# Kernel tuning notes

Hardware: AMD Instinct MI355X
Metric: run time of the kernel (lower is better)

Reference implementation:

```python
import jax, jax.numpy as jnp
import numpy as np

BN_EPS = 1e-5


def setup_inputs() -> dict:
    key = jax.random.key(0)
    ks = jax.random.split(key, 12)
    N, F, H, E, ED, G, EMB = 59392, 116, 256, 950272, 5, 8, 16
    return {
        "x": jax.random.normal(ks[0], (N, F), dtype=jnp.float32),
        "edge_index": jax.random.randint(ks[1], (2, E), 0, N, dtype=jnp.int64),
        "edge_attr": jax.random.normal(ks[2], (E, ED), dtype=jnp.float32),
        "group_ids": jax.random.randint(ks[3], (N,), 0, G, dtype=jnp.int64),
        "group_emb": jax.random.normal(ks[4], (G, EMB), dtype=jnp.float32),
        "W_in": jax.random.normal(ks[5], (F + EMB, H), dtype=jnp.float32) * 0.05,
        "b_in": jnp.zeros((H,), dtype=jnp.float32),
        "gamma": jnp.ones((H,), dtype=jnp.float32),
        "beta": jnp.zeros((H,), dtype=jnp.float32),
        "We": jax.random.normal(ks[6], (ED, H), dtype=jnp.float32) * 0.05,
        "be": jnp.zeros((H,), dtype=jnp.float32),
        "W1": jax.random.normal(ks[7], (H, H), dtype=jnp.float32) * 0.05,
        "b1": jnp.zeros((H,), dtype=jnp.float32),
        "W2": jax.random.normal(ks[8], (H, H), dtype=jnp.float32) * 0.05,
        "b2": jnp.zeros((H,), dtype=jnp.float32),
    }


def reference(x, edge_index, edge_attr, group_ids, group_emb, W_in, b_in,
              gamma, beta, We, be, W1, b1, W2, b2):
    N = x.shape[0]
    # group-embedding concat (dropout is identity in eval mode)
    h = jnp.concatenate([x, group_emb[group_ids]], axis=-1)      # [N, F+EMB]
    # dynamically-created Linear + ReLU
    h = jax.nn.relu(h @ W_in + b_in)                              # [N, H]
    # BatchNorm over nodes (training stats, biased var)
    mu = jnp.mean(h, axis=0)
    var = jnp.mean(jnp.square(h - mu), axis=0)
    h = (h - mu) * jax.lax.rsqrt(var + BN_EPS) * gamma + beta
    # GINEConv: msg = ReLU(x_j + lin(edge_attr)); sum-aggregate at target
    src, dst = edge_index[0], edge_index[1]
    msg = jax.nn.relu(h[src] + edge_attr @ We + be)               # [E, H]
    agg = jax.ops.segment_sum(msg, dst, num_segments=N)          # [N, H]
    z = h + agg                                                   # (1+eps)*h, eps=0
    out = jax.nn.relu(z @ W1 + b1) @ W2 + b2                      # 2-layer MLP
    out = jax.nn.relu(out)
    return (out, edge_attr)
```

## Files before the change

kernel.cpp:

```cpp
#include <hip/hip_runtime.h>
#include <hip/hip_bf16.h>
#include <cstdint>
#include <cstddef>

#define H 256
#define EMB 16
#define ED 5
#define BN_EPS 1e-5f
#define CAP 48

typedef __attribute__((ext_vector_type(8))) short short8;
typedef __attribute__((ext_vector_type(4))) float f32x4;
typedef _Float16 h2 __attribute__((ext_vector_type(2)));

__device__ __forceinline__ unsigned short f2bf(float f) {
  unsigned int u = __float_as_uint(f);
  unsigned int r = (u + 0x7fffu + ((u >> 16) & 1u)) >> 16;
  return (unsigned short)r;
}
__device__ __forceinline__ unsigned int pk2bf(float a, float b) {
  return (unsigned int)f2bf(a) | ((unsigned int)f2bf(b) << 16);
}
__device__ __forceinline__ unsigned short f2h(float f) {
  union { _Float16 h; unsigned short u; } c;
  c.h = (_Float16)f;
  return c.u;
}
__device__ __forceinline__ h2 u2h2(unsigned int u) {
  union { unsigned int u; h2 h; } c;
  c.u = u;
  return c.h;
}
__device__ __forceinline__ unsigned int h22u(h2 h) {
  union { h2 h; unsigned int u; } c;
  c.h = h;
  return c.u;
}
__device__ __forceinline__ h2 mkh2(float a, float b) {
  h2 r;
  r.x = (_Float16)a;
  r.y = (_Float16)b;
  return r;
}

__global__ __launch_bounds__(256) void prep_kernel(
    const float* __restrict__ Win, const float* __restrict__ W1,
    const float* __restrict__ W2, const float* __restrict__ gemb,
    const float* __restrict__ b_in, unsigned short* __restrict__ Wtx,
    unsigned short* __restrict__ Wt1, unsigned short* __restrict__ Wt2,
    float* __restrict__ T, float* __restrict__ stats, int* __restrict__ cnt,
    int N, int F, int G) {
  int idx = blockIdx.x * 256 + threadIdx.x;
  if (idx < 1024) stats[idx] = 0.f;
  if (idx < N) cnt[idx] = 0;
  if (idx < 256 * 128) {
    int n = idx >> 7, k = idx & 127;
    Wtx[idx] = f2bf((k < F) ? Win[(size_t)k * H + n] : 0.f);
  } else if (idx < 256 * 128 + 65536) {
    int i2 = idx - 256 * 128;
    int n = i2 >> 8, k = i2 & 255;
    Wt1[i2] = f2bf(W1[(size_t)k * H + n]);
  } else if (idx < 256 * 128 + 131072) {
    int i2 = idx - 256 * 128 - 65536;
    int n = i2 >> 8, k = i2 & 255;
    Wt2[i2] = f2bf(W2[(size_t)k * H + n]);
  } else if (idx < 256 * 128 + 131072 + G * 256) {
    int i2 = idx - 256 * 128 - 131072;
    int g = i2 >> 8, c = i2 & 255;
    float s = b_in[c];
    #pragma unroll
    for (int k = 0; k < EMB; ++k)
      s = fmaf(gemb[g * EMB + k], Win[(size_t)(F + k) * H + c], s);
    T[i2] = s;
  }
}

__global__ __launch_bounds__(256) void gemm_in_kernel(
    const float* __restrict__ x, const int* __restrict__ gid,
    const unsigned short* __restrict__ Wtx, const float* __restrict__ T,
    unsigned short* __restrict__ h0, float* __restrict__ stats, int F) {
  const int m0 = blockIdx.y * 128;
  const int n0 = blockIdx.x * 128;
  const int tid = threadIdx.x;
  const int lane = tid & 63;
  const int wave = tid >> 6;
  const int wm = (wave & 1) * 64;
  const int wn = (wave >> 1) * 64;
  const int l16 = lane & 15;
  const int quad = lane >> 4;
  __shared__ __align__(16) unsigned short As[128][40];
  __shared__ __align__(16) unsigned short Bs[128][40];
  __shared__ float cs[128], css[128];
  if (tid < 128) {
    cs[tid] = 0.f;
    css[tid] = 0.f;
  }
  f32x4 acc[4][4] = {};
  const int srow = tid >> 1;
  const int half = tid & 1;
  for (int k0 = 0; k0 < 128; k0 += 32) {
    __syncthreads();
    {
      const float* xp = x + (size_t)(m0 + srow) * F;
      float4 xv[4];
      #pragma unroll
      for (int f = 0; f < 4; ++f) {
        int c = k0 + half * 16 + f * 4;
        xv[f] = (c < F) ? *(const float4*)(xp + c)
                        : make_float4(0.f, 0.f, 0.f, 0.f);
      }
      uint4 p0, p1;
      p0.x = pk2bf(xv[0].x, xv[0].y); p0.y = pk2bf(xv[0].z, xv[0].w);
      p0.z = pk2bf(xv[1].x, xv[1].y); p0.w = pk2bf(xv[1].z, xv[1].w);
      p1.x = pk2bf(xv[2].x, xv[2].y); p1.y = pk2bf(xv[2].z, xv[2].w);
      p1.z = pk2bf(xv[3].x, xv[3].y); p1.w = pk2bf(xv[3].z, xv[3].w);
      *(uint4*)(&As[srow][half * 16]) = p0;
      *(uint4*)(&As[srow][half * 16 + 8]) = p1;
    }
    {
      const unsigned short* wp = Wtx + (size_t)(n0 + srow) * 128 + k0 + half * 16;
      *(uint4*)(&Bs[srow][half * 16]) = *(const uint4*)wp;
      *(uint4*)(&Bs[srow][half * 16 + 8]) = *(const uint4*)(wp + 8);
    }
    __syncthreads();
    short8 af[4], bf[4];
    #pragma unroll
    for (int i = 0; i < 4; ++i)
      af[i] = *(const short8*)(&As[wm + i * 16 + l16][quad * 8]);
    #pragma unroll
    for (int j = 0; j < 4; ++j)
      bf[j] = *(const short8*)(&Bs[wn + j * 16 + l16][quad * 8]);
    #pragma unroll
    for (int i = 0; i < 4; ++i)
      #pragma unroll
      for (int j = 0; j < 4; ++j)
        acc[i][j] = __builtin_amdgcn_mfma_f32_16x16x32_bf16(af[i], bf[j],
                                                            acc[i][j], 0, 0, 0);
  }
  int gi[4][4];
  #pragma unroll
  for (int i = 0; i < 4; ++i)
    #pragma unroll
    for (int r = 0; r < 4; ++r)
      gi[i][r] = gid[m0 + wm + i * 16 + quad * 4 + r];
  float ls[4] = {}, lss[4] = {};
  #pragma unroll
  for (int j = 0; j < 4; ++j) {
    const int col = n0 + wn + j * 16 + l16;
    #pragma unroll
    for (int i = 0; i < 4; ++i) {
      #pragma unroll
      for (int r = 0; r < 4; ++r) {
        const int row = m0 + wm + i * 16 + quad * 4 + r;
        float v = fmaxf(acc[i][j][r] + T[gi[i][r] * H + col], 0.f);
        h0[(size_t)row * H + col] = f2h(v);
        ls[j] += v;
        lss[j] = fmaf(v, v, lss[j]);
      }
    }
  }
  #pragma unroll
  for (int j = 0; j < 4; ++j) {
    const int lc = wn + j * 16 + l16;
    atomicAdd(&cs[lc], ls[j]);
    atomicAdd(&css[lc], lss[j]);
  }
  __syncthreads();
  if (tid < 128) {
    atomicAdd(&stats[n0 + tid], cs[tid]);
    atomicAdd(&stats[H + n0 + tid], css[tid]);
  }
}

__global__ __launch_bounds__(256) void mlp_kernel(
    const unsigned short* __restrict__ z, const unsigned short* __restrict__ Wt1,
    const unsigned short* __restrict__ Wt2, const float* __restrict__ b1,
    const float* __restrict__ b2, float* __restrict__ out) {
  const int m0 = blockIdx.x * 64;
  const int tid = threadIdx.x;
  const int lane = tid & 63;
  const int wave = tid >> 6;
  const int wn = wave * 64;
  const int l16 = lane & 15;
  const int quad = lane >> 4;
  __shared__ __align__(16) unsigned short As[64][40];
  __shared__ __align__(16) unsigned short Bs[256][40];
  __shared__ __align__(16) unsigned short hidS[64][264];
  f32x4 acc[4][4] = {};
  const int ar = tid >> 2, ac = tid & 3;
  for (int k0 = 0; k0 < 256; k0 += 32) {
    __syncthreads();
    *(float4*)(&As[ar][ac * 8]) =
        *(const float4*)(z + (size_t)(m0 + ar) * H + k0 + ac * 8);
    #pragma unroll
    for (int t = 0; t < 4; ++t) {
      int r = ar + t * 64;
      *(float4*)(&Bs[r][ac * 8]) =
          *(const float4*)(Wt1 + (size_t)r * H + k0 + ac * 8);
    }
    __syncthreads();
    short8 af[4], bf[4];
    #pragma unroll
    for (int i = 0; i < 4; ++i)
      af[i] = *(const short8*)(&As[i * 16 + l16][quad * 8]);
    #pragma unroll
    for (int j = 0; j < 4; ++j)
      bf[j] = *(const short8*)(&Bs[wn + j * 16 + l16][quad * 8]);
    #pragma unroll
    for (int i = 0; i < 4; ++i)
      #pragma unroll
      for (int j = 0; j < 4; ++j)
        acc[i][j] = __builtin_amdgcn_mfma_f32_16x16x32_bf16(af[i], bf[j],
                                                            acc[i][j], 0, 0, 0);
  }
  #pragma unroll
  for (int j = 0; j < 4; ++j) {
    const int col = wn + j * 16 + l16;
    const float bj = b1[col];
    #pragma unroll
    for (int i = 0; i < 4; ++i)
      #pragma unroll
      for (int r = 0; r < 4; ++r) {
        const int row = i * 16 + quad * 4 + r;
        hidS[row][col] = f2bf(fmaxf(acc[i][j][r] + bj, 0.f));
      }
  }
  #pragma unroll
  for (int i = 0; i < 4; ++i)
    #pragma unroll
    for (int j = 0; j < 4; ++j)
      acc[i][j] = (f32x4){0.f, 0.f, 0.f, 0.f};
  for (int k0 = 0; k0 < 256; k0 += 32) {
    __syncthreads();
    #pragma unroll
    for (int t = 0; t < 4; ++t) {
      int r = ar + t * 64;
      *(float4*)(&Bs[r][ac * 8]) =
          *(const float4*)(Wt2 + (size_t)r * H + k0 + ac * 8);
    }
    __syncthreads();
    short8 af[4], bf[4];
    #pragma unroll
    for (int i = 0; i < 4; ++i)
      af[i] = *(const short8*)(&hidS[i * 16 + l16][k0 + quad * 8]);
    #pragma unroll
    for (int j = 0; j < 4; ++j)
      bf[j] = *(const short8*)(&Bs[wn + j * 16 + l16][quad * 8]);
    #pragma unroll
    for (int i = 0; i < 4; ++i)
      #pragma unroll
      for (int j = 0; j < 4; ++j)
        acc[i][j] = __builtin_amdgcn_mfma_f32_16x16x32_bf16(af[i], bf[j],
                                                            acc[i][j], 0, 0, 0);
  }
  #pragma unroll
  for (int j = 0; j < 4; ++j) {
    const int col = wn + j * 16 + l16;
    const float bj = b2[col];
    #pragma unroll
    for (int i = 0; i < 4; ++i)
      #pragma unroll
      for (int r = 0; r < 4; ++r) {
        const int row = m0 + i * 16 + quad * 4 + r;
        out[(size_t)row * H + col] = fmaxf(acc[i][j][r] + bj, 0.f);
      }
  }
}

__global__ __launch_bounds__(256) void csr_scatter_kernel(
    const int* __restrict__ ei, const float* __restrict__ ea,
    int* __restrict__ cnt, uint4* __restrict__ rec,
    float* __restrict__ ea_out, int E) {
  int e = blockIdx.x * 256 + threadIdx.x;
  if (e >= E) return;
  int s = ei[e];
  int d = ei[E + e];
  const float* eap = ea + (size_t)e * ED;
  const float e0 = eap[0], e1 = eap[1], e2 = eap[2], e3 = eap[3], e4 = eap[4];
  int p = atomicAdd(&cnt[d], 1);
  if (p >= CAP) p = CAP - 1;
  uint4 r;
  r.x = ((unsigned)s) << 9;
  r.y = h22u(mkh2(e0, e1));
  r.z = h22u(mkh2(e2, e3));
  r.w = h22u(mkh2(e4, 0.f));
  rec[(size_t)d * CAP + p] = r;
  float* op = ea_out + (size_t)e * ED;
  op[0] = e0; op[1] = e1; op[2] = e2; op[3] = e3; op[4] = e4;
}

__device__ __forceinline__ void edge_accum(
    const uint4 rr, const uint2 hv, const h2 aA, const h2 aB,
    const h2 bA, const h2 bB, const h2 wA[5], const h2 wB[5],
    float& ax, float& ay, float& az, float& aw) {
  h2 m01 = aA * u2h2(hv.x) + bA;
  h2 m23 = aB * u2h2(hv.y) + bB;
  const h2 e01 = u2h2(rr.y), e23 = u2h2(rr.z), e44 = u2h2(rr.w);
  h2 t;
  t.x = e01.x; t.y = e01.x;  m01 += t * wA[0]; m23 += t * wB[0];
  t.x = e01.y; t.y = e01.y;  m01 += t * wA[1]; m23 += t * wB[1];
  t.x = e23.x; t.y = e23.x;  m01 += t * wA[2]; m23 += t * wB[2];
  t.x = e23.y; t.y = e23.y;  m01 += t * wA[3]; m23 += t * wB[3];
  t.x = e44.x; t.y = e44.x;  m01 += t * wA[4]; m23 += t * wB[4];
  const h2 z2 = {(_Float16)0.f, (_Float16)0.f};
  m01 = __builtin_elementwise_max(m01, z2);
  m23 = __builtin_elementwise_max(m23, z2);
  ax += (float)m01.x;
  ay += (float)m01.y;
  az += (float)m23.x;
  aw += (float)m23.y;
}

__global__ __launch_bounds__(256) void aggregate_kernel(
    const unsigned short* __restrict__ h0, const uint4* __restrict__ rec,
    const float* __restrict__ We, const float* __restrict__ be,
    const float* __restrict__ gamma, const float* __restrict__ beta,
    const float* __restrict__ stats, const int* __restrict__ cntv,
    unsigned short* __restrict__ z, int N, float inv_n) {
  const int lane = threadIdx.x & 63;
  int n = blockIdx.x * 4 + (threadIdx.x >> 6);
  if (n >= N) return;
  n = __builtin_amdgcn_readfirstlane(n);
  const int c = lane * 4;
  const int c2 = c << 1;
  const float4 be4 = *(const float4*)(be + c);
  h2 aA, aB, bA, bB;
  {
    const float4 s1v = *(const float4*)(stats + c);
    const float4 s2v = *(const float4*)(stats + H + c);
    const float4 g4 = *(const float4*)(gamma + c);
    const float4 bt4 = *(const float4*)(beta + c);
    float a[4], b[4];
    float m0 = s1v.x * inv_n, m1 = s1v.y * inv_n,
          m2 = s1v.z * inv_n, m3 = s1v.w * inv_n;
    a[0] = g4.x / sqrtf(s2v.x * inv_n - m0 * m0 + BN_EPS);
    a[1] = g4.y / sqrtf(s2v.y * inv_n - m1 * m1 + BN_EPS);
    a[2] = g4.z / sqrtf(s2v.z * inv_n - m2 * m2 + BN_EPS);
    a[3] = g4.w / sqrtf(s2v.w * inv_n - m3 * m3 + BN_EPS);
    b[0] = bt4.x - m0 * a[0] + be4.x;
    b[1] = bt4.y - m1 * a[1] + be4.y;
    b[2] = bt4.z - m2 * a[2] + be4.z;
    b[3] = bt4.w - m3 * a[3] + be4.w;
    aA = mkh2(a[0], a[1]); aB = mkh2(a[2], a[3]);
    bA = mkh2(b[0], b[1]); bB = mkh2(b[2], b[3]);
  }
  h2 wA[5], wB[5];
  #pragma unroll
  for (int k = 0; k < 5; ++k) {
    wA[k] = mkh2(We[k * H + c], We[k * H + c + 1]);
    wB[k] = mkh2(We[k * H + c + 2], We[k * H + c + 3]);
  }
  float ax = 0.f, ay = 0.f, az = 0.f, aw = 0.f;
  int cnt = __builtin_amdgcn_readfirstlane(cntv[n]);
  cnt = (cnt < CAP) ? cnt : CAP;
  const uint4* rp = rec + (size_t)n * CAP;
  const char* hb = (const char*)h0;
  int i = 0;
  for (; i + 8 <= cnt; i += 8) {
    uint4 rr[8];
    uint2 hh[8];
    #pragma unroll
    for (int u = 0; u < 8; ++u) rr[u] = rp[i + u];
    #pragma unroll
    for (int u = 0; u < 8; ++u)
      hh[u] = *(const uint2*)(hb + rr[u].x + c2);
    #pragma unroll
    for (int u = 0; u < 8; ++u)
      edge_accum(rr[u], hh[u], aA, aB, bA, bB, wA, wB, ax, ay, az, aw);
  }
  for (; i + 4 <= cnt; i += 4) {
    uint4 rr[4];
    uint2 hh[4];
    #pragma unroll
    for (int u = 0; u < 4; ++u) rr[u] = rp[i + u];
    #pragma unroll
    for (int u = 0; u < 4; ++u)
      hh[u] = *(const uint2*)(hb + rr[u].x + c2);
    #pragma unroll
    for (int u = 0; u < 4; ++u)
      edge_accum(rr[u], hh[u], aA, aB, bA, bB, wA, wB, ax, ay, az, aw);
  }
  for (; i < cnt; ++i) {
    const uint4 r0 = rp[i];
    const uint2 h0v = *(const uint2*)(hb + r0.x + c2);
    edge_accum(r0, h0v, aA, aB, bA, bB, wA, wB, ax, ay, az, aw);
  }
  const uint2 hs = *(const uint2*)(h0 + (size_t)n * H + c);
  const h2 s01 = aA * u2h2(hs.x) + bA;
  const h2 s23 = aB * u2h2(hs.y) + bB;
  float zx = (float)s01.x - be4.x + ax;
  float zy = (float)s01.y - be4.y + ay;
  float zz = (float)s23.x - be4.z + az;
  float zw = (float)s23.y - be4.w + aw;
  uint2 o;
  o.x = pk2bf(zx, zy);
  o.y = pk2bf(zz, zw);
  *(uint2*)(z + (size_t)n * H + c) = o;
}

extern "C" void kernel_launch(void* const* d_in, const int* in_sizes, int n_in,
                              void* d_out, int out_size, void* d_ws, size_t ws_size,
                              hipStream_t stream) {
  const float* x     = (const float*)d_in[0];
  const int*   ei    = (const int*)d_in[1];
  const float* ea    = (const float*)d_in[2];
  const int*   gid   = (const int*)d_in[3];
  const float* gemb  = (const float*)d_in[4];
  const float* W_in  = (const float*)d_in[5];
  const float* b_in  = (const float*)d_in[6];
  const float* gamma = (const float*)d_in[7];
  const float* beta  = (const float*)d_in[8];
  const float* We    = (const float*)d_in[9];
  const float* be    = (const float*)d_in[10];
  const float* W1    = (const float*)d_in[11];
  const float* b1    = (const float*)d_in[12];
  const float* W2    = (const float*)d_in[13];
  const float* b2    = (const float*)d_in[14];
  float* out = (float*)d_out;

  const int N = in_sizes[3];
  const int E = in_sizes[1] / 2;
  const int F = in_sizes[0] / N;
  const int G = in_sizes[4] / EMB;

  char* p = (char*)d_ws;
  auto take = [&](size_t bytes) {
    char* r = p;
    p += (bytes + 255) & ~(size_t)255;
    return r;
  };
  float* stats          = (float*)take(1024 * sizeof(float));
  int* cnt              = (int*)take((size_t)N * 4);
  uint4* rec            = (uint4*)take((size_t)N * CAP * 16);
  unsigned short* Wtx   = (unsigned short*)take((size_t)256 * 128 * 2);
  unsigned short* Wt1   = (unsigned short*)take((size_t)H * H * 2);
  unsigned short* Wt2   = (unsigned short*)take((size_t)H * H * 2);
  float* T              = (float*)take((size_t)G * H * 4);
  unsigned short* h0    = (unsigned short*)take((size_t)N * H * 2);
  unsigned short* z     = (unsigned short*)take((size_t)N * H * 2);

  {
    int total = 256 * 128 + 131072 + G * 256;
    int nb = (total + 255) / 256;
    if (nb < (N + 255) / 256) nb = (N + 255) / 256;
    prep_kernel<<<nb, 256, 0, stream>>>(W_in, W1, W2, gemb, b_in, Wtx, Wt1,
                                        Wt2, T, stats, cnt, N, F, G);
  }

  csr_scatter_kernel<<<(E + 255) / 256, 256, 0, stream>>>(
      ei, ea, cnt, rec, out + (size_t)N * H, E);

  dim3 ggrid(H / 128, N / 128);
  gemm_in_kernel<<<ggrid, 256, 0, stream>>>(x, gid, Wtx, T, h0, stats, F);

  aggregate_kernel<<<(N + 3) / 4, 256, 0, stream>>>(
      h0, rec, We, be, gamma, beta, stats, cnt, z, N, 1.0f / (float)N);

  mlp_kernel<<<N / 64, 256, 0, stream>>>(z, Wt1, Wt2, b1, b2, out);
}
```

Baseline: 334.5 us.

## Fuse edge scatter and input GEMM into one interleaved launch

Merges the CSR edge-scatter kernel and the input-projection GEMM kernel into a single launch. Block ids are interleaved so every fifth block does a GEMM tile and the rest do scatter work. The aim is to overlap the memory/atomic-bound scatter with the compute-bound GEMM and save a kernel boundary. The cost is that all blocks carry the GEMM's shared-memory footprint, which may reduce occupancy for the scatter blocks.

```diff
diff --git a/kernel.cpp b/kernel.cpp
--- a/kernel.cpp
+++ b/kernel.cpp
@@ -75,22 +75,51 @@
   }
 }
 
-__global__ __launch_bounds__(256) void gemm_in_kernel(
+__global__ __launch_bounds__(256) void scatter_gemm_kernel(
+    const int* __restrict__ ei, const float* __restrict__ ea,
+    int* __restrict__ cnt, uint4* __restrict__ rec,
+    float* __restrict__ ea_out, int E,
     const float* __restrict__ x, const int* __restrict__ gid,
     const unsigned short* __restrict__ Wtx, const float* __restrict__ T,
-    unsigned short* __restrict__ h0, float* __restrict__ stats, int F) {
-  const int m0 = blockIdx.y * 128;
-  const int n0 = blockIdx.x * 128;
+    unsigned short* __restrict__ h0, float* __restrict__ stats,
+    int F, int GB) {
+  __shared__ __align__(16) unsigned short As[128][40];
+  __shared__ __align__(16) unsigned short Bs[128][40];
+  __shared__ float cs[128], css[128];
+  const int bid = blockIdx.x;
   const int tid = threadIdx.x;
+  const bool isG = ((bid % 5) == 4) && (bid / 5 < GB);
+  if (!isG) {
+    const int nG = min((bid + 1) / 5, GB);
+    const int sb = bid - nG;
+    int e = sb * 256 + tid;
+    if (e >= E) return;
+    int s = ei[e];
+    int d = ei[E + e];
+    const float* eap = ea + (size_t)e * ED;
+    const float e0 = eap[0], e1 = eap[1], e2 = eap[2], e3 = eap[3],
+                e4 = eap[4];
+    int p = atomicAdd(&cnt[d], 1);
+    if (p >= CAP) p = CAP - 1;
+    uint4 r;
+    r.x = ((unsigned)s) << 9;
+    r.y = h22u(mkh2(e0, e1));
+    r.z = h22u(mkh2(e2, e3));
+    r.w = h22u(mkh2(e4, 0.f));
+    rec[(size_t)d * CAP + p] = r;
+    float* op = ea_out + (size_t)e * ED;
+    op[0] = e0; op[1] = e1; op[2] = e2; op[3] = e3; op[4] = e4;
+    return;
+  }
+  const int gidx = bid / 5;
+  const int m0 = (gidx >> 1) * 128;
+  const int n0 = (gidx & 1) * 128;
   const int lane = tid & 63;
   const int wave = tid >> 6;
   const int wm = (wave & 1) * 64;
   const int wn = (wave >> 1) * 64;
   const int l16 = lane & 15;
   const int quad = lane >> 4;
-  __shared__ __align__(16) unsigned short As[128][40];
-  __shared__ __align__(16) unsigned short Bs[128][40];
-  __shared__ float cs[128], css[128];
   if (tid < 128) {
     cs[tid] = 0.f;
     css[tid] = 0.f;
@@ -265,28 +294,6 @@
         out[(size_t)row * H + col] = fmaxf(acc[i][j][r] + bj, 0.f);
       }
   }
-}
-
-__global__ __launch_bounds__(256) void csr_scatter_kernel(
-    const int* __restrict__ ei, const float* __restrict__ ea,
-    int* __restrict__ cnt, uint4* __restrict__ rec,
-    float* __restrict__ ea_out, int E) {
-  int e = blockIdx.x * 256 + threadIdx.x;
-  if (e >= E) return;
-  int s = ei[e];
-  int d = ei[E + e];
-  const float* eap = ea + (size_t)e * ED;
-  const float e0 = eap[0], e1 = eap[1], e2 = eap[2], e3 = eap[3], e4 = eap[4];
-  int p = atomicAdd(&cnt[d], 1);
-  if (p >= CAP) p = CAP - 1;
-  uint4 r;
-  r.x = ((unsigned)s) << 9;
-  r.y = h22u(mkh2(e0, e1));
-  r.z = h22u(mkh2(e2, e3));
-  r.w = h22u(mkh2(e4, 0.f));
-  rec[(size_t)d * CAP + p] = r;
-  float* op = ea_out + (size_t)e * ED;
-  op[0] = e0; op[1] = e1; op[2] = e2; op[3] = e3; op[4] = e4;
 }
 
 __device__ __forceinline__ void edge_accum(
@@ -447,11 +454,13 @@
                                         Wt2, T, stats, cnt, N, F, G);
   }
 
-  csr_scatter_kernel<<<(E + 255) / 256, 256, 0, stream>>>(
-      ei, ea, cnt, rec, out + (size_t)N * H, E);
-
-  dim3 ggrid(H / 128, N / 128);
-  gemm_in_kernel<<<ggrid, 256, 0, stream>>>(x, gid, Wtx, T, h0, stats, F);
+  {
+    const int SB = (E + 255) / 256;
+    const int GB = (N / 128) * (H / 128);
+    scatter_gemm_kernel<<<SB + GB, 256, 0, stream>>>(
+        ei, ea, cnt, rec, out + (size_t)N * H, E,
+        x, gid, Wtx, T, h0, stats, F, GB);
+  }
 
   aggregate_kernel<<<(N + 3) / 4, 256, 0, stream>>>(
       h0, rec, We, be, gamma, beta, stats, cnt, z, N, 1.0f / (float)N);
```

Measured after the change: 321.3 us. 1.04x faster.
